# Kernel tuning notes

Measured on AMD Instinct MI355X. Metric: run time of the kernel, lower is better.

## Reference

```python
import jax, jax.numpy as jnp
import numpy as np

B, S, D, H = 4, 2048, 1024, 16
HS = D // H  # head size = 64


def setup_inputs() -> dict:
    key = jax.random.key(0)
    k1, k2, k3 = jax.random.split(key, 3)
    return {
        "input_data": jax.random.normal(k1, (B, S, D), dtype=jnp.float32),
        "w_qkv": jax.random.normal(k2, (D, 3 * D), dtype=jnp.float32) * (1.0 / np.sqrt(D)),
        "b_qkv": jnp.zeros((3 * D,), dtype=jnp.float32),
        "w_proj": jax.random.normal(k3, (D, D), dtype=jnp.float32) * (1.0 / np.sqrt(D)),
        "b_proj": jnp.zeros((D,), dtype=jnp.float32),
    }


def reference(input_data, w_qkv, b_qkv, w_proj, b_proj):
    b, s, d = input_data.shape
    qkv = input_data @ w_qkv + b_qkv  # [b, s, 3d]
    q, k, v = jnp.split(qkv, 3, axis=-1)
    # [b, h, s, hs]
    q = q.reshape(b, s, H, HS).transpose(0, 2, 1, 3)
    k = k.reshape(b, s, H, HS).transpose(0, 2, 1, 3)
    v = v.reshape(b, s, H, HS).transpose(0, 2, 1, 3)
    # NB: original module scales by 1/sqrt(num_heads), not 1/sqrt(head_size)
    scores = jnp.einsum('bhqd,bhkd->bhqk', q, k) / jnp.sqrt(jnp.float32(H))
    causal = jnp.tril(jnp.ones((s, s), dtype=bool))
    scores = jnp.where(causal[None, None], scores, -jnp.inf)
    weights = jax.nn.softmax(scores, axis=-1)  # dropout p=0.0 -> identity
    out = jnp.einsum('bhqk,bhkd->bhqd', weights, v)
    out = out.transpose(0, 2, 1, 3).reshape(b, s, d)
    return out @ w_proj + b_proj
```

## Files before the change

kernel.cpp:

```cpp
#include <hip/hip_runtime.h>


typedef unsigned short u16;
typedef short bf16x8 __attribute__((ext_vector_type(8)));
typedef unsigned short u16x8 __attribute__((ext_vector_type(8)));
typedef float f32x4 __attribute__((ext_vector_type(4)));
typedef float f32x16 __attribute__((ext_vector_type(16)));

#define S_LEN 2048
#define DMODEL 1024
#define NHEAD 16
#define MROWS 8192

#define SCALE_LOG2E 0.36067376022224085f
#define DEFER_THR 8.0f

__device__ __forceinline__ u16 f2bf(float f) {
  union { float f; unsigned u; } c; c.f = f;
  unsigned u = c.u;
  u += 0x7fffu + ((u >> 16) & 1u);
  return (u16)(u >> 16);
}

__device__ __forceinline__ float exp2_fast(float x) {
  float r; asm("v_exp_f32 %0, %1" : "=v"(r) : "v"(x)); return r;
}

__device__ __forceinline__ unsigned cvtpk_bf16(float a, float b) {
  unsigned r;
  asm("v_cvt_pk_bf16_f32 %0, %1, %2" : "=v"(r) : "v"(a), "v"(b));
  return r;
}

__device__ __forceinline__ void plswap(unsigned& a, unsigned& b) {
  asm("v_permlane32_swap_b32 %0, %1" : "+v"(a), "+v"(b));
}

__device__ __forceinline__ f32x4 mfma16(bf16x8 a, bf16x8 b, f32x4 c) {
  return __builtin_amdgcn_mfma_f32_16x16x32_bf16(a, b, c, 0, 0, 0);
}

__device__ __forceinline__ f32x16 mfma32(bf16x8 a, bf16x8 b, f32x16 c) {
  return __builtin_amdgcn_mfma_f32_32x32x16_bf16(a, b, c, 0, 0, 0);
}

__device__ __forceinline__ void gload_lds16(const void* g, void* l) {
  __builtin_amdgcn_global_load_lds((__attribute__((address_space(1))) void*)g,
                                   (__attribute__((address_space(3))) void*)l,
                                   16, 0, 0);
}

__global__ void k_f32_to_bf16(const float* __restrict__ in, u16* __restrict__ out, int n) {
  int i = (blockIdx.x * 256 + threadIdx.x) * 4;
  if (i < n) {
    float4 v = *reinterpret_cast<const float4*>(in + i);
    ushort4 o;
    o.x = f2bf(v.x); o.y = f2bf(v.y); o.z = f2bf(v.z); o.w = f2bf(v.w);
    *reinterpret_cast<ushort4*>(out + i) = o;
  }
}

__global__ void k_transpose_to_bf16(const float* __restrict__ in, u16* __restrict__ out,
                                    int K, int N) {
  __shared__ float t[32][33];
  int n0 = blockIdx.x * 32, k0 = blockIdx.y * 32;
  int tx = threadIdx.x & 31, ty = threadIdx.x >> 5;
#pragma unroll
  for (int i = 0; i < 32; i += 8)
    t[ty + i][tx] = in[(size_t)(k0 + ty + i) * N + n0 + tx];
  __syncthreads();
#pragma unroll
  for (int i = 0; i < 32; i += 8)
    out[(size_t)(n0 + ty + i) * K + k0 + tx] = f2bf(t[tx][ty + i]);
}

template <int MODE>
__global__ __launch_bounds__(512, 1) void k_gemm8(const u16* __restrict__ A,
                                                  const u16* __restrict__ Bt,
                                                  const float* __restrict__ bias,
                                                  u16* __restrict__ outb,
                                                  float* __restrict__ outf,
                                                  u16* __restrict__ vtout,
                                                  int N, int K) {
  __shared__ u16 As[2][2][256 * 32];
  __shared__ u16 Bs[2][2][128 * 32];

  const int tid = threadIdx.x;
  const int lane = tid & 63, wave = tid >> 6;
  const int wr = wave >> 1, wc = wave & 1;
  const int lr = lane & 15, lk = lane >> 4;
  const int m0 = blockIdx.x * 256, n0 = blockIdx.y * 128;
  const size_t Kb = (size_t)K * 2;

  const int csw = ((tid & 3) ^ ((tid >> 3) & 3)) * 16;
  const char* Asrc0 = (const char*)A + (size_t)(m0 + (tid >> 2)) * Kb + csw;
  const char* Asrc1 = Asrc0 + 128 * Kb;
  const char* Bsrc0 = (const char*)Bt + (size_t)(n0 + (tid >> 2)) * Kb + csw;

#define STAGE_KH(BUFX, KH, T)                                                  \
  {                                                                            \
    const size_t ko_ = (size_t)(T) * 128 + (KH) * 64;                          \
    gload_lds16(Asrc0 + ko_, &As[BUFX][KH][(size_t)tid * 8]);                  \
    gload_lds16(Asrc1 + ko_, &As[BUFX][KH][((size_t)tid + 512) * 8]);          \
    gload_lds16(Bsrc0 + ko_, &Bs[BUFX][KH][(size_t)tid * 8]);                  \
  }

  f32x4 zero4 = {0.f, 0.f, 0.f, 0.f};
  f32x4 acc[4][4];
#pragma unroll
  for (int m = 0; m < 4; ++m)
#pragma unroll
    for (int n = 0; n < 4; ++n) acc[m][n] = zero4;

  const int slotsw = (lr >> 1) & 3;

#define PHASE(BUFX, KH, T, DOSTAGE, VMZERO)                                    \
  {                                                                            \
    if (VMZERO) asm volatile("s_waitcnt vmcnt(0)" ::: "memory");               \
    else        asm volatile("s_waitcnt vmcnt(3)" ::: "memory");               \
    __builtin_amdgcn_s_barrier();                                              \
    __builtin_amdgcn_sched_barrier(0);                                         \
    bf16x8 af[4], bfr[4];                                                      \
    _Pragma("unroll") for (int m = 0; m < 4; ++m)                              \
        af[m] = *reinterpret_cast<const bf16x8*>(                              \
            &As[BUFX][KH][(wr * 64 + m * 16 + lr) * 32 + ((lk ^ slotsw) * 8)]);\
    _Pragma("unroll") for (int n = 0; n < 4; ++n)                              \
        bfr[n] = *reinterpret_cast<const bf16x8*>(                             \
            &Bs[BUFX][KH][(wc * 64 + n * 16 + lr) * 32 + ((lk ^ slotsw) * 8)]);\
    if (DOSTAGE) STAGE_KH((BUFX) ^ 1, KH, (T) + 1);                            \
    __builtin_amdgcn_sched_barrier(0);                                         \
    __builtin_amdgcn_s_setprio(1);                                             \
    _Pragma("unroll") for (int m = 0; m < 4; ++m)                              \
        _Pragma("unroll") for (int n = 0; n < 4; ++n)                          \
            acc[m][n] = mfma16(af[m], bfr[n], acc[m][n]);                      \
    __builtin_amdgcn_s_setprio(0);                                             \
  }

  const int nkt = K >> 6;
  STAGE_KH(0, 0, 0);
  STAGE_KH(0, 1, 0);

  for (int t = 0; t < nkt - 1; ++t) {
    const int buf = t & 1;
    PHASE(buf, 0, t, 1, 0);
    PHASE(buf, 1, t, 1, 0);
  }
  {
    const int buf = (nkt - 1) & 1;
    PHASE(buf, 0, nkt - 1, 0, 0);
    PHASE(buf, 1, nkt - 1, 0, 1);
  }
#undef PHASE
#undef STAGE_KH

#pragma unroll
  for (int n = 0; n < 4; ++n) {
    int col = n0 + wc * 64 + n * 16 + lr;
    float bv = bias[col];
#pragma unroll
    for (int m = 0; m < 4; ++m) {
      int rowb = m0 + wr * 64 + m * 16 + lk * 4;
      if (MODE == 1) {
#pragma unroll
        for (int r = 0; r < 4; ++r)
          outf[(size_t)(rowb + r) * N + col] = acc[m][n][r] + bv;
      } else {
        if (col < 2048) {
          const float qs = (col < 1024) ? SCALE_LOG2E : 1.0f;
#pragma unroll
          for (int r = 0; r < 4; ++r)
            outb[(size_t)(rowb + r) * 2048 + col] = f2bf((acc[m][n][r] + bv) * qs);
        } else {
          int hh = (col >> 6) & 15, dd = col & 63;
          int bb = rowb >> 11, ss = rowb & 2047;
          ushort4 o;
          o.x = f2bf(acc[m][n][0] + bv);
          o.y = f2bf(acc[m][n][1] + bv);
          o.z = f2bf(acc[m][n][2] + bv);
          o.w = f2bf(acc[m][n][3] + bv);
          *reinterpret_cast<ushort4*>(
              vtout + ((size_t)(bb * 16 + hh) * 64 + dd) * 2048 + ss) = o;
        }
      }
    }
  }
}

__global__ __launch_bounds__(256, 4) void k_attn6(const u16* __restrict__ qk,
                                                  const u16* __restrict__ vt,
                                                  u16* __restrict__ ao) {
  __shared__ u16 Ks[2][4096];
  __shared__ u16 Vs[2][4096];

  const int tid = threadIdx.x;
  const int lane = tid & 63, wave = tid >> 6;
  const int l31 = lane & 31, hi = lane >> 5;
  const int gid = blockIdx.x;
  const int bh = gid & 63;
  const int tq = gid >> 6;
  const int g2 = tq >> 2, r2 = tq & 3;
  const int qt = (g2 == 0) ? 2 * r2
               : (g2 == 1) ? 15 - 2 * r2
               : (g2 == 2) ? 2 * r2 + 1
                           : 14 - 2 * r2;
  const int b = bh >> 4, h = bh & 15;

  const int q0 = qt * 128 + wave * 32;
  const int ktd = (q0 + 31) >> 6;
  const int KTMAX = 2 * qt + 1;
  const int qrel = q0 + l31 - ktd * 64;

  bf16x8 qf[4];
  {
    const u16* qp = qk + ((size_t)b * S_LEN + q0 + l31) * 2048 + h * 64 + hi * 8;
#pragma unroll
    for (int ks = 0; ks < 4; ++ks)
      qf[ks] = *reinterpret_cast<const bf16x8*>(qp + ks * 16);
  }

  const int swzcol = 16 * ((lane & 7) ^ (lane >> 3));
  const char* kg = (const char*)qk + ((size_t)b * S_LEN) * 4096 + 2048 + h * 128 +
                   (size_t)(lane >> 3) * 4096 + swzcol;
  const char* vg = (const char*)vt + ((size_t)bh * 64 + (lane >> 3)) * 4096 + swzcol;

#define STAGE(BUF, KT)                                                              \
  {                                                                                 \
    const char* kg_ = kg + (size_t)(KT) * 64 * 4096;                                \
    const char* vg_ = vg + (size_t)(KT) * 128;                                      \
    gload_lds16(kg_ + (size_t)(wave * 8) * 4096, &Ks[BUF][wave * 512]);             \
    gload_lds16(kg_ + (size_t)((wave + 4) * 8) * 4096, &Ks[BUF][(wave + 4) * 512]); \
    gload_lds16(vg_ + (size_t)(wave * 8) * 4096, &Vs[BUF][wave * 512]);             \
    gload_lds16(vg_ + (size_t)((wave + 4) * 8) * 4096, &Vs[BUF][(wave + 4) * 512]); \
  }

  f32x16 oT[2];
#pragma unroll
  for (int kb = 0; kb < 2; ++kb)
#pragma unroll
    for (int g = 0; g < 16; ++g) oT[kb][g] = 0.f;
  float m_i = -INFINITY;
  float l_i = 0.f;

  const int rsw = (l31 & 7) << 4;

  STAGE(0, 0);
  __syncthreads();
  int buf = 0;

  for (int kt = 0; kt <= KTMAX; ++kt) {
    if (kt < KTMAX) STAGE(buf ^ 1, kt + 1);

    if (kt <= ktd) {
      const char* Kb = (const char*)&Ks[buf][0];
      const char* Vb = (const char*)&Vs[buf][0];
      const bool masked = (kt == ktd);

      bf16x8 kf[2][4];
#pragma unroll
      for (int kb = 0; kb < 2; ++kb)
#pragma unroll
        for (int ks = 0; ks < 4; ++ks)
          kf[kb][ks] = *reinterpret_cast<const bf16x8*>(
              Kb + (kb * 32 + l31) * 128 + ((ks * 32 + hi * 16) ^ rsw));

      f32x16 sc[2];
#pragma unroll
      for (int kb = 0; kb < 2; ++kb) {
        sc[kb] = mfma32(kf[kb][0], qf[0], f32x16{});
#pragma unroll
        for (int ks = 1; ks < 4; ++ks) sc[kb] = mfma32(kf[kb][ks], qf[ks], sc[kb]);
      }

      bf16x8 vf[2][4];
#pragma unroll
      for (int kbd = 0; kbd < 2; ++kbd)
#pragma unroll
        for (int t = 0; t < 4; ++t)
          vf[kbd][t] = *reinterpret_cast<const bf16x8*>(
              Vb + (kbd * 32 + l31) * 128 + ((t * 32 + hi * 16) ^ rsw));

      if (masked) {
#pragma unroll
        for (int kb = 0; kb < 2; ++kb)
#pragma unroll
          for (int g = 0; g < 16; ++g) {
            int key_ = kb * 32 + (g & 3) + ((g >> 2) << 3) + hi * 4;
            if (key_ > qrel) sc[kb][g] = -INFINITY;
          }
      }
      float mxa = fmaxf(sc[0][0], sc[0][4]), mxb = fmaxf(sc[0][1], sc[0][5]);
      float mxc = fmaxf(sc[0][2], sc[0][6]), mxd = fmaxf(sc[0][3], sc[0][7]);
#pragma unroll
      for (int g = 8; g < 16; g += 4) {
        mxa = fmaxf(mxa, sc[0][g]);     mxb = fmaxf(mxb, sc[0][g + 1]);
        mxc = fmaxf(mxc, sc[0][g + 2]); mxd = fmaxf(mxd, sc[0][g + 3]);
      }
#pragma unroll
      for (int g = 0; g < 16; g += 4) {
        mxa = fmaxf(mxa, sc[1][g]);     mxb = fmaxf(mxb, sc[1][g + 1]);
        mxc = fmaxf(mxc, sc[1][g + 2]); mxd = fmaxf(mxd, sc[1][g + 3]);
      }
      float mx = fmaxf(fmaxf(mxa, mxb), fmaxf(mxc, mxd));
      mx = fmaxf(mx, __shfl_xor(mx, 32, 64));
      if (__any(mx > m_i + DEFER_THR)) {
        float mn = fmaxf(m_i, mx);
        float c = exp2_fast(m_i - mn);
        m_i = mn;
        l_i *= c;
#pragma unroll
        for (int kb = 0; kb < 2; ++kb)
#pragma unroll
          for (int g = 0; g < 16; ++g) oT[kb][g] *= c;
      }
      float rsa = 0.f, rsb = 0.f, rsc = 0.f, rsd = 0.f;
      unsigned pk_[8][2];
#pragma unroll
      for (int kb = 0; kb < 2; ++kb)
#pragma unroll
        for (int s = 0; s < 4; ++s) {
          float p0 = exp2_fast(sc[kb][s * 4 + 0] - m_i);
          float p1 = exp2_fast(sc[kb][s * 4 + 1] - m_i);
          float p2 = exp2_fast(sc[kb][s * 4 + 2] - m_i);
          float p3 = exp2_fast(sc[kb][s * 4 + 3] - m_i);
          rsa += p0; rsb += p1; rsc += p2; rsd += p3;
          pk_[kb * 4 + s][0] = cvtpk_bf16(p0, p1);
          pk_[kb * 4 + s][1] = cvtpk_bf16(p2, p3);
        }
      float rs = (rsa + rsb) + (rsc + rsd);
      rs += __shfl_xor(rs, 32, 64);
      l_i += rs;

      bf16x8 pfr[4];
#pragma unroll
      for (int t = 0; t < 4; ++t) {
        unsigned a0 = pk_[2 * t][0], b0 = pk_[2 * t + 1][0];
        unsigned a1 = pk_[2 * t][1], b1 = pk_[2 * t + 1][1];
        plswap(a0, b0);
        plswap(a1, b1);
        unsigned fr[4] = {a0, a1, b0, b1};
        pfr[t] = *reinterpret_cast<const bf16x8*>(&fr[0]);
      }

#pragma unroll
      for (int t = 0; t < 4; ++t) {
        oT[0] = mfma32(vf[0][t], pfr[t], oT[0]);
        oT[1] = mfma32(vf[1][t], pfr[t], oT[1]);
      }
    }

    __syncthreads();
    buf ^= 1;
  }
#undef STAGE

  {
    float inv = 1.f / l_i;
    u16* orow = ao + ((size_t)b * S_LEN + q0 + l31) * DMODEL + h * 64 + hi * 4;
#pragma unroll
    for (int kbd = 0; kbd < 2; ++kbd)
#pragma unroll
      for (int s = 0; s < 4; ++s) {
        unsigned w0 = cvtpk_bf16(oT[kbd][s * 4 + 0] * inv, oT[kbd][s * 4 + 1] * inv);
        unsigned w1 = cvtpk_bf16(oT[kbd][s * 4 + 2] * inv, oT[kbd][s * 4 + 3] * inv);
        *reinterpret_cast<unsigned*>(orow + kbd * 32 + s * 8) = w0;
        *reinterpret_cast<unsigned*>(orow + kbd * 32 + s * 8 + 2) = w1;
      }
  }
}

extern "C" void kernel_launch(void* const* d_in, const int* in_sizes, int n_in,
                              void* d_out, int out_size, void* d_ws, size_t ws_size,
                              hipStream_t stream) {
  const float* x = (const float*)d_in[0];
  const float* wqkv = (const float*)d_in[1];
  const float* bqkv = (const float*)d_in[2];
  const float* wproj = (const float*)d_in[3];
  const float* bproj = (const float*)d_in[4];
  float* out = (float*)d_out;

  char* ws = (char*)d_ws;
  u16* Xb     = (u16*)(ws);
  u16* Wqkvt  = (u16*)(ws + (size_t)16777216);
  u16* Wprojt = (u16*)(ws + (size_t)23068672);
  u16* QKb    = (u16*)(ws + (size_t)25165824);
  u16* Vt     = (u16*)(ws + (size_t)58720256);
  u16* AOb    = (u16*)(ws + (size_t)75497472);

  k_f32_to_bf16<<<MROWS * DMODEL / 4 / 256, 256, 0, stream>>>(x, Xb, MROWS * DMODEL);
  k_transpose_to_bf16<<<dim3(3072 / 32, 1024 / 32), 256, 0, stream>>>(wqkv, Wqkvt, 1024, 3072);
  k_transpose_to_bf16<<<dim3(1024 / 32, 1024 / 32), 256, 0, stream>>>(wproj, Wprojt, 1024, 1024);

  k_gemm8<2><<<dim3(MROWS / 256, 3072 / 128), 512, 0, stream>>>(
      Xb, Wqkvt, bqkv, QKb, nullptr, Vt, 3072, 1024);

  k_attn6<<<dim3(1024), 256, 0, stream>>>(QKb, Vt, AOb);

  k_gemm8<1><<<dim3(MROWS / 256, DMODEL / 128), 512, 0, stream>>>(
      AOb, Wprojt, bproj, nullptr, out, nullptr, DMODEL, 1024);
}
```

Measured before the change: 191.6 us.

## Grow attention blocks to 8 waves covering 256 query rows

The attention kernel now launches 512 blocks of 512 threads, each handling 256 query rows with 8 waves sharing the same staged K/V tiles, instead of 1024 blocks of 256 threads over 128 rows. Each wave now issues one K and one V async load per tile rather than two of each. This halves the global-to-LDS traffic per query and simplifies the causal load-balancing order to a paired mapping of 8 tiles. In exchange, blocks are larger and fewer, and waves within a block do uneven amounts of work near the diagonal, which can leave more idle time at barriers.

```diff
diff --git a/kernel.cpp b/kernel.cpp
--- a/kernel.cpp
+++ b/kernel.cpp
@@ -186,7 +186,7 @@
   }
 }
 
-__global__ __launch_bounds__(256, 4) void k_attn6(const u16* __restrict__ qk,
+__global__ __launch_bounds__(512, 4) void k_attn7(const u16* __restrict__ qk,
                                                   const u16* __restrict__ vt,
                                                   u16* __restrict__ ao) {
   __shared__ u16 Ks[2][4096];
@@ -198,16 +198,12 @@
   const int gid = blockIdx.x;
   const int bh = gid & 63;
   const int tq = gid >> 6;
-  const int g2 = tq >> 2, r2 = tq & 3;
-  const int qt = (g2 == 0) ? 2 * r2
-               : (g2 == 1) ? 15 - 2 * r2
-               : (g2 == 2) ? 2 * r2 + 1
-                           : 14 - 2 * r2;
+  const int t = (tq < 4) ? tq : 11 - tq;
   const int b = bh >> 4, h = bh & 15;
 
-  const int q0 = qt * 128 + wave * 32;
+  const int q0 = t * 256 + wave * 32;
   const int ktd = (q0 + 31) >> 6;
-  const int KTMAX = 2 * qt + 1;
+  const int KTMAX = 4 * t + 3;
   const int qrel = q0 + l31 - ktd * 64;
 
   bf16x8 qf[4];
@@ -220,17 +216,14 @@
 
   const int swzcol = 16 * ((lane & 7) ^ (lane >> 3));
   const char* kg = (const char*)qk + ((size_t)b * S_LEN) * 4096 + 2048 + h * 128 +
-                   (size_t)(lane >> 3) * 4096 + swzcol;
-  const char* vg = (const char*)vt + ((size_t)bh * 64 + (lane >> 3)) * 4096 + swzcol;
-
-#define STAGE(BUF, KT)                                                              \
-  {                                                                                 \
-    const char* kg_ = kg + (size_t)(KT) * 64 * 4096;                                \
-    const char* vg_ = vg + (size_t)(KT) * 128;                                      \
-    gload_lds16(kg_ + (size_t)(wave * 8) * 4096, &Ks[BUF][wave * 512]);             \
-    gload_lds16(kg_ + (size_t)((wave + 4) * 8) * 4096, &Ks[BUF][(wave + 4) * 512]); \
-    gload_lds16(vg_ + (size_t)(wave * 8) * 4096, &Vs[BUF][wave * 512]);             \
-    gload_lds16(vg_ + (size_t)((wave + 4) * 8) * 4096, &Vs[BUF][(wave + 4) * 512]); \
+                   (size_t)(wave * 8 + (lane >> 3)) * 4096 + swzcol;
+  const char* vg = (const char*)vt +
+                   ((size_t)bh * 64 + wave * 8 + (lane >> 3)) * 4096 + swzcol;
+
+#define STAGE(BUF, KT)                                                   \
+  {                                                                      \
+    gload_lds16(kg + (size_t)(KT) * 64 * 4096, &Ks[BUF][wave * 512]);    \
+    gload_lds16(vg + (size_t)(KT) * 128, &Vs[BUF][wave * 512]);          \
   }
 
   f32x16 oT[2];
@@ -275,9 +268,9 @@
 #pragma unroll
       for (int kbd = 0; kbd < 2; ++kbd)
 #pragma unroll
-        for (int t = 0; t < 4; ++t)
-          vf[kbd][t] = *reinterpret_cast<const bf16x8*>(
-              Vb + (kbd * 32 + l31) * 128 + ((t * 32 + hi * 16) ^ rsw));
+        for (int tt = 0; tt < 4; ++tt)
+          vf[kbd][tt] = *reinterpret_cast<const bf16x8*>(
+              Vb + (kbd * 32 + l31) * 128 + ((tt * 32 + hi * 16) ^ rsw));
 
       if (masked) {
 #pragma unroll
@@ -332,19 +325,19 @@
 
       bf16x8 pfr[4];
 #pragma unroll
-      for (int t = 0; t < 4; ++t) {
-        unsigned a0 = pk_[2 * t][0], b0 = pk_[2 * t + 1][0];
-        unsigned a1 = pk_[2 * t][1], b1 = pk_[2 * t + 1][1];
+      for (int tt = 0; tt < 4; ++tt) {
+        unsigned a0 = pk_[2 * tt][0], b0 = pk_[2 * tt + 1][0];
+        unsigned a1 = pk_[2 * tt][1], b1 = pk_[2 * tt + 1][1];
         plswap(a0, b0);
         plswap(a1, b1);
         unsigned fr[4] = {a0, a1, b0, b1};
-        pfr[t] = *reinterpret_cast<const bf16x8*>(&fr[0]);
-      }
-
-#pragma unroll
-      for (int t = 0; t < 4; ++t) {
-        oT[0] = mfma32(vf[0][t], pfr[t], oT[0]);
-        oT[1] = mfma32(vf[1][t], pfr[t], oT[1]);
+        pfr[tt] = *reinterpret_cast<const bf16x8*>(&fr[0]);
+      }
+
+#pragma unroll
+      for (int tt = 0; tt < 4; ++tt) {
+        oT[0] = mfma32(vf[0][tt], pfr[tt], oT[0]);
+        oT[1] = mfma32(vf[1][tt], pfr[tt], oT[1]);
       }
     }
 
@@ -393,7 +386,7 @@
   k_gemm8<2><<<dim3(MROWS / 256, 3072 / 128), 512, 0, stream>>>(
       Xb, Wqkvt, bqkv, QKb, nullptr, Vt, 3072, 1024);
 
-  k_attn6<<<dim3(1024), 256, 0, stream>>>(QKb, Vt, AOb);
+  k_attn7<<<dim3(512), 512, 0, stream>>>(QKb, Vt, AOb);
 
   k_gemm8<1><<<dim3(MROWS / 256, DMODEL / 128), 512, 0, stream>>>(
       AOb, Wprojt, bproj, nullptr, out, nullptr, DMODEL, 1024);
```

After: 186.4 us. 2.7% less time.
